# Kernel tuning notes

Hardware: AMD Instinct MI355X
Metric: run time of the kernel (lower is better)

The kernel has to match this reference:

```python
import jax, jax.numpy as jnp
import numpy as np

GROUPS = 32
GN_EPS = 1e-6
LN_EPS = 1e-5
HEADS = 8
DH = 40


def group_norm(x, w, b):
    # x: [B, C, H, W], GroupNorm over (C//GROUPS, H, W) within each group
    B, C, H, W = x.shape
    xg = x.reshape(B, GROUPS, C // GROUPS, H, W)
    mu = xg.mean(axis=(2, 3, 4), keepdims=True)
    var = xg.var(axis=(2, 3, 4), keepdims=True)
    xg = (xg - mu) * jax.lax.rsqrt(var + GN_EPS)
    return xg.reshape(B, C, H, W) * w[None, :, None, None] + b[None, :, None, None]


def layer_norm(x, w, b):
    mu = x.mean(axis=-1, keepdims=True)
    var = x.var(axis=-1, keepdims=True)
    return (x - mu) * jax.lax.rsqrt(var + LN_EPS) * w + b


def attention(x, ctx, wq, wk, wv, wo, bo):
    # x: [B, N, D], ctx: [B, M, Dc]; weights stored (in, out)
    B, N, _ = x.shape
    M = ctx.shape[1]
    q = (x @ wq).reshape(B, N, HEADS, DH)
    k = (ctx @ wk).reshape(B, M, HEADS, DH)
    v = (ctx @ wv).reshape(B, M, HEADS, DH)
    sim = jnp.einsum('bihd,bjhd->bhij', q, k) * (DH ** -0.5)
    attn = jax.nn.softmax(sim, axis=-1)
    out = jnp.einsum('bhij,bjhd->bihd', attn, v).reshape(B, N, HEADS * DH)
    return out @ wo + bo


def geglu_ff(x, w1, b1, w2, b2):
    h = x @ w1 + b1
    a, g = jnp.split(h, 2, axis=-1)
    return (a * jax.nn.gelu(g, approximate=False)) @ w2 + b2


def conv1x1(x, w, b):
    # w: [C_out, C_in]
    return jnp.einsum('bihw,oi->bohw', x, w) + b[None, :, None, None]


def reference(x, context, gn_w, gn_b, pin_w, pin_b,
              ln1_w, ln1_b, q1, k1, v1, o1_w, o1_b,
              ln2_w, ln2_b, q2, k2, v2, o2_w, o2_b,
              ln3_w, ln3_b, ff1_w, ff1_b, ff2_w, ff2_b,
              pout_w, pout_b):
    B, C, H, W = x.shape
    x_in = x
    h = group_norm(x, gn_w, gn_b)
    h = conv1x1(h, pin_w, pin_b)
    h = h.reshape(B, C, H * W).transpose(0, 2, 1)  # b (h w) c
    # BasicTransformerBlock
    h = attention(layer_norm(h, ln1_w, ln1_b), layer_norm(h, ln1_w, ln1_b), q1, k1, v1, o1_w, o1_b) + h
    h = attention(layer_norm(h, ln2_w, ln2_b), context, q2, k2, v2, o2_w, o2_b) + h
    h = geglu_ff(layer_norm(h, ln3_w, ln3_b), ff1_w, ff1_b, ff2_w, ff2_b) + h
    h = h.transpose(0, 2, 1).reshape(B, C, H, W)
    h = conv1x1(h, pout_w, pout_b)
    return h + x_in


def setup_inputs() -> dict:
    key = jax.random.key(0)
    ks = jax.random.split(key, 20)
    B, C, H, W = 1, 320, 64, 64
    CTX_N, CTX_D = 77, 768
    INNER, FFI = 320, 1280

    def n(k, shape, s=0.02):
        return jax.random.normal(k, shape, jnp.float32) * s

    return {
        'x': jax.random.normal(ks[0], (B, C, H, W), jnp.float32),
        'context': jax.random.normal(ks[1], (B, CTX_N, CTX_D), jnp.float32),
        'gn_w': jnp.ones((C,), jnp.float32), 'gn_b': jnp.zeros((C,), jnp.float32),
        'pin_w': n(ks[2], (INNER, C)), 'pin_b': jnp.zeros((INNER,), jnp.float32),
        'ln1_w': jnp.ones((INNER,), jnp.float32), 'ln1_b': jnp.zeros((INNER,), jnp.float32),
        'q1': n(ks[3], (INNER, INNER)), 'k1': n(ks[4], (INNER, INNER)), 'v1': n(ks[5], (INNER, INNER)),
        'o1_w': n(ks[6], (INNER, INNER)), 'o1_b': jnp.zeros((INNER,), jnp.float32),
        'ln2_w': jnp.ones((INNER,), jnp.float32), 'ln2_b': jnp.zeros((INNER,), jnp.float32),
        'q2': n(ks[7], (INNER, INNER)), 'k2': n(ks[8], (CTX_D, INNER)), 'v2': n(ks[9], (CTX_D, INNER)),
        'o2_w': n(ks[10], (INNER, INNER)), 'o2_b': jnp.zeros((INNER,), jnp.float32),
        'ln3_w': jnp.ones((INNER,), jnp.float32), 'ln3_b': jnp.zeros((INNER,), jnp.float32),
        'ff1_w': n(ks[11], (INNER, 2 * FFI)), 'ff1_b': jnp.zeros((2 * FFI,), jnp.float32),
        'ff2_w': n(ks[12], (FFI, INNER)), 'ff2_b': jnp.zeros((INNER,), jnp.float32),
        'pout_w': n(ks[13], (C, INNER)), 'pout_b': jnp.zeros((C,), jnp.float32),
    }
```

## Files before the change

kernel.cpp:

```cpp
#include <hip/hip_runtime.h>
#include <hip/hip_bf16.h>
#include <math.h>

#define N_SEQ  4096
#define DMODEL 320
#define NHEADS 8
#define DHEAD  40
#define CTXN   77
#define CTXD   768
#define FFI    1280

typedef short s8v __attribute__((ext_vector_type(8)));
typedef short s4v __attribute__((ext_vector_type(4)));
typedef float f4v __attribute__((ext_vector_type(4)));
typedef unsigned short u16;

static __device__ __forceinline__ u16 bf16u(float x) {
    unsigned u = __float_as_uint(x);
    return (u16)((u + 0x7FFFu + ((u >> 16) & 1u)) >> 16);
}
static __device__ __forceinline__ float b2f(u16 v) { return __uint_as_float((unsigned)v << 16); }
static __device__ __forceinline__ unsigned pack2(float a, float b) {
    return (unsigned)bf16u(a) | ((unsigned)bf16u(b) << 16);
}

#define GLD_LDS16(gp, lp) __builtin_amdgcn_global_load_lds( \
    (const __attribute__((address_space(1))) void*)(gp),    \
    (__attribute__((address_space(3))) void*)(lp), 16, 0, 0)

struct WC { const float* s; u16* d; int K, O, trans; };
struct WCs { WC a[12]; };
__global__ __launch_bounds__(256) void wcast2_k(WCs P) {
    __shared__ float tile[32][33];
    WC w = P.a[blockIdx.y];
    if (w.trans) {
        int ntk = w.K >> 5, nto = w.O >> 5;
        int tid = blockIdx.x;
        if (tid >= ntk * nto) return;
        int tk = tid % ntk, to = tid / ntk;
        int lr = threadIdx.x >> 5, lc = threadIdx.x & 31;
#pragma unroll
        for (int p = 0; p < 4; ++p) {
            int k = tk * 32 + p * 8 + lr;
            tile[p * 8 + lr][lc] = w.s[(size_t)k * w.O + to * 32 + lc];
        }
        __syncthreads();
#pragma unroll
        for (int p = 0; p < 4; ++p) {
            int o = to * 32 + p * 8 + lr;
            w.d[(size_t)o * w.K + tk * 32 + lc] = bf16u(tile[lc][p * 8 + lr]);
        }
    } else {
        int nel = w.K * w.O;
        for (int e = blockIdx.x * 256 + threadIdx.x; e < nel; e += gridDim.x * 256)
            w.d[e] = bf16u(w.s[e]);
    }
}

__global__ __launch_bounds__(256) void gn_stats_k(const float* __restrict__ x,
                                                  const float* __restrict__ gw, const float* __restrict__ gb,
                                                  float* __restrict__ sc, float* __restrict__ sh) {
    __shared__ float red[512];
    __shared__ float ms[2];
    int g = blockIdx.x, t = threadIdx.x;
    const float* xp = x + (size_t)g * 40960;
    float s = 0.f, ss = 0.f;
    for (int i = t; i < 40960; i += 256) { float v = xp[i]; s += v; ss += v * v; }
    red[t] = s; red[256 + t] = ss;
    __syncthreads();
    for (int st = 128; st > 0; st >>= 1) {
        if (t < st) { red[t] += red[t + st]; red[256 + t] += red[256 + t + st]; }
        __syncthreads();
    }
    if (t == 0) {
        float mean = red[0] / 40960.f;
        float var  = red[256] / 40960.f - mean * mean;
        ms[0] = mean; ms[1] = rsqrtf(var + 1e-6f);
    }
    __syncthreads();
    if (t < 10) {
        int c = g * 10 + t;
        float scv = gw[c] * ms[1];
        sc[c] = scv;
        sh[c] = gb[c] - ms[0] * scv;
    }
}

__global__ __launch_bounds__(256) void ln_stats_k(const float* __restrict__ in,
                                                  float* __restrict__ mu, float* __restrict__ rs) {
    int row = blockIdx.x * 4 + (threadIdx.x >> 6), l = threadIdx.x & 63;
    const float* p = in + (size_t)row * DMODEL;
    float s = 0.f, ss = 0.f;
#pragma unroll
    for (int j = 0; j < 5; ++j) { float v = p[l + 64 * j]; s += v; ss += v * v; }
    for (int o = 32; o > 0; o >>= 1) { s += __shfl_xor(s, o); ss += __shfl_xor(ss, o); }
    if (l == 0) {
        float mean = s * (1.f / 320.f);
        float var  = ss * (1.f / 320.f) - mean * mean;
        mu[row] = mean;
        rs[row] = rsqrtf(var + 1e-5f);
    }
}

struct GArg { const u16* Wt; const float* bias; float* outf; u16* outb; int ob_mode; };
#define GP 72
#define QSCALE 0.22811012f

template<int SITE>
__global__ __launch_bounds__(256) void gemm_t(const void* __restrict__ Av, int a_mode, int lda,
                                              const float* __restrict__ mu, const float* __restrict__ rs,
                                              const float* __restrict__ cw, const float* __restrict__ cb,
                                              GArg g0, GArg g1, GArg g2,
                                              const float* __restrict__ res,
                                              int Mrows, int K, int Oout, int obT_stride) {
    __shared__ __align__(16) u16 As[2][64 * GP];
    __shared__ __align__(16) u16 Wsm[2][64 * 64];
    const int t = threadIdx.x;
    const int w = t >> 6, lane = t & 63, c = lane & 15, quad = lane >> 4;
    const int o0 = blockIdx.x * 64, n0 = blockIdx.y * 64;
    GArg g = (blockIdx.z == 0) ? g0 : ((blockIdx.z == 1) ? g1 : g2);
    const f4v zero = {0.f, 0.f, 0.f, 0.f};
    f4v acc[4] = {zero, zero, zero, zero};
    const s8v z8 = {0, 0, 0, 0, 0, 0, 0, 0};
    const int nk = K >> 6;

    float fA[16];
    s8v bA0 = z8, bA1 = z8;

    const u16* gW0 = g.Wt + (size_t)(o0 + w * 16 + (lane >> 3)) * K + ((lane & 7) ^ (lane >> 3)) * 8;
    const u16* gW1 = gW0 + (size_t)8 * K;
    const int wdst = w * 1024;
    const int swb0 = 8 * (quad ^ (c & 7));
    const int swb1 = 8 * ((quad + 4) ^ (c & 7));

    auto gllW = [&](int b) {
        GLD_LDS16(gW0, &Wsm[b][wdst]);
        GLD_LDS16(gW1, &Wsm[b][wdst + 512]);
        gW0 += 64; gW1 += 64;
    };
    auto loadA = [&](int k0) {
        if (a_mode == 0) {
            const u16* A = (const u16*)Av;
            int i0 = t, i1 = t + 256;
            int nA = n0 + (i0 >> 3), nB = n0 + (i1 >> 3);
            bA0 = (nA < Mrows) ? *(const s8v*)(A + (size_t)nA * lda + k0 + (i0 & 7) * 8) : z8;
            bA1 = (nB < Mrows) ? *(const s8v*)(A + (size_t)nB * lda + k0 + (i1 & 7) * 8) : z8;
        } else if (a_mode == 1) {
            const float* A = (const float*)Av;
            int r = t >> 2, s16 = (t & 3) * 16;
            int n = n0 + r;
            if (n < Mrows) {
                const float* src = A + (size_t)n * lda + k0 + s16;
#pragma unroll
                for (int i = 0; i < 16; ++i) fA[i] = src[i];
            } else {
#pragma unroll
                for (int i = 0; i < 16; ++i) fA[i] = 0.f;
            }
        } else if (a_mode == 2) {
            const float* A = (const float*)Av;
#pragma unroll
            for (int j = 0; j < 16; ++j) {
                int e = t + 256 * j; int nn = e & 63, kk = e >> 6;
                int n = n0 + nn, kgl = k0 + kk;
                fA[j] = (n < Mrows) ? A[(size_t)kgl * lda + n] * cw[kgl] + cb[kgl] : 0.f;
            }
        } else if (a_mode == 3) {
            const float* A = (const float*)Av;
            int r = t >> 2, s16 = (t & 3) * 16;
            int n = n0 + r;
            if (n < Mrows) {
                const float* src = A + (size_t)n * lda + k0 + s16;
                const float* cwp = cw + k0 + s16;
                const float* cbp = cb + k0 + s16;
                float m_ = mu[n], rr = rs[n];
#pragma unroll
                for (int i = 0; i < 16; ++i) fA[i] = (src[i] - m_) * rr * cwp[i] + cbp[i];
            } else {
#pragma unroll
                for (int i = 0; i < 16; ++i) fA[i] = 0.f;
            }
        } else {
            const u16* Op = (const u16*)Av;
            const float* lp = mu;
            int r = t >> 2, s16 = (t & 3) * 16;
            int n = n0 + r;
            int ch0 = k0 + s16;
            int hdA = ch0 / 40;
            int hdB = (ch0 + 15) / 40;
            float invA = 1.f / (lp[(size_t)hdA * N_SEQ + n] + lp[(size_t)(8 + hdA) * N_SEQ + n]);
            float invB = (hdB == hdA) ? invA
                       : 1.f / (lp[(size_t)hdB * N_SEQ + n] + lp[(size_t)(8 + hdB) * N_SEQ + n]);
#pragma unroll
            for (int i = 0; i < 16; ++i) {
                int ch = ch0 + i;
                int hd = ch / 40;
                int d  = ch - hd * 40;
                float num = b2f(Op[((size_t)hd * N_SEQ + n) * DHEAD + d])
                          + b2f(Op[((size_t)(8 + hd) * N_SEQ + n) * DHEAD + d]);
                fA[i] = num * ((hd == hdA) ? invA : invB);
            }
        }
    };
    auto storeA = [&](int b) {
        if (a_mode == 0) {
            int i0 = t, i1 = t + 256;
            *(s8v*)&As[b][(i0 >> 3) * GP + (i0 & 7) * 8] = bA0;
            *(s8v*)&As[b][(i1 >> 3) * GP + (i1 & 7) * 8] = bA1;
        } else if (a_mode == 2) {
#pragma unroll
            for (int j = 0; j < 16; ++j) {
                int e = t + 256 * j; int nn = e & 63, kk = e >> 6;
                As[b][nn * GP + kk] = bf16u(fA[j]);
            }
        } else {
            int r = t >> 2, s16 = (t & 3) * 16;
            unsigned* dst = (unsigned*)&As[b][r * GP + s16];
#pragma unroll
            for (int i = 0; i < 8; ++i) dst[i] = pack2(fA[2 * i], fA[2 * i + 1]);
        }
    };

    gllW(0); loadA(0);
    storeA(0);
    __syncthreads();
    for (int k = 0; k < nk; ++k) {
        const int cur = k & 1;
        if (k + 1 < nk) { gllW(1 - cur); loadA((k + 1) << 6); }
        s8v a0 = *(const s8v*)&As[cur][(w * 16 + c) * GP + quad * 8];
        s8v a1 = *(const s8v*)&As[cur][(w * 16 + c) * GP + 32 + quad * 8];
#pragma unroll
        for (int nt = 0; nt < 4; ++nt) {
            s8v b0 = *(const s8v*)&Wsm[cur][(nt * 16 + c) * 64 + swb0];
            s8v b1 = *(const s8v*)&Wsm[cur][(nt * 16 + c) * 64 + swb1];
            acc[nt] = __builtin_amdgcn_mfma_f32_16x16x32_bf16(a0, b0, acc[nt], 0, 0, 0);
            acc[nt] = __builtin_amdgcn_mfma_f32_16x16x32_bf16(a1, b1, acc[nt], 0, 0, 0);
        }
        if (k + 1 < nk) { storeA(1 - cur); }
        __syncthreads();
    }
#pragma unroll
    for (int nt = 0; nt < 4; ++nt) {
        int o = o0 + nt * 16 + c;
        float vv[4];
#pragma unroll
        for (int r = 0; r < 4; ++r) vv[r] = acc[nt][r] + (g.bias ? g.bias[o] : 0.f);
        if (g.ob_mode == 3) {
            int nb = n0 + w * 16 + quad * 4;
            const float4 x4 = *(const float4*)(res + (size_t)o * obT_stride + nb);
            float4 o4 = make_float4(vv[0] + x4.x, vv[1] + x4.y, vv[2] + x4.z, vv[3] + x4.w);
            *(float4*)(g.outf + (size_t)o * obT_stride + nb) = o4;
        } else if (g.ob_mode == 4) {
#pragma unroll
            for (int r = 0; r < 4; ++r) {
                int n = n0 + w * 16 + quad * 4 + r;
                float vvv = vv[r];
                if (o < 320) vvv *= QSCALE;
                u16 bv = bf16u(vvv);
                if (o < 320)      g0.outb[(size_t)n * 320 + o] = bv;
                else if (o < 640) g1.outb[(size_t)n * 320 + (o - 320)] = bv;
                else              g2.outb[(size_t)(o - 640) * obT_stride + n] = bv;
            }
        } else {
#pragma unroll
            for (int r = 0; r < 4; ++r) {
                int n = n0 + w * 16 + quad * 4 + r;
                if (n >= Mrows) continue;
                float v = vv[r];
                if (res) v += res[(size_t)n * Oout + o];
                if (g.outf) g.outf[(size_t)n * Oout + o] = v;
                if (g.ob_mode == 1) g.outb[(size_t)n * Oout + o] = bf16u(v);
                else if (g.ob_mode == 2) g.outb[(size_t)o * obT_stride + n] = bf16u(v);
            }
        }
    }
}

__global__ __launch_bounds__(256) void gemm_gg(const float* __restrict__ A, int lda,
                                               const float* __restrict__ mu, const float* __restrict__ rs,
                                               const float* __restrict__ cw, const float* __restrict__ cb,
                                               const u16* __restrict__ Wt, const float* __restrict__ bias,
                                               u16* __restrict__ outb,
                                               int K, int Oout, int geglu_off) {
    __shared__ __align__(16) u16 As[64 * GP];
    __shared__ __align__(16) u16 Wsm[64 * GP];
    __shared__ __align__(16) u16 Wgm[64 * GP];
    const int t = threadIdx.x;
    const int w = t >> 6, lane = t & 63, c = lane & 15, quad = lane >> 4;
    const int o0 = blockIdx.x * 64, n0 = blockIdx.y * 64;
    const f4v zero = {0.f, 0.f, 0.f, 0.f};
    f4v acc[4]  = {zero, zero, zero, zero};
    f4v accg[4] = {zero, zero, zero, zero};
    const int nk = K >> 6;

    float fA[16];
    s8v wv0, wv1, gv0, gv1;

    auto loadWG = [&](int k0) {
        int i0 = t, i1 = t + 256;
        wv0 = *(const s8v*)(Wt + (size_t)(o0 + (i0 >> 3)) * K + k0 + (i0 & 7) * 8);
        wv1 = *(const s8v*)(Wt + (size_t)(o0 + (i1 >> 3)) * K + k0 + (i1 & 7) * 8);
        gv0 = *(const s8v*)(Wt + (size_t)(o0 + (i0 >> 3) + geglu_off) * K + k0 + (i0 & 7) * 8);
        gv1 = *(const s8v*)(Wt + (size_t)(o0 + (i1 >> 3) + geglu_off) * K + k0 + (i1 & 7) * 8);
    };
    auto storeWG = [&]() {
        int i0 = t, i1 = t + 256;
        *(s8v*)&Wsm[(i0 >> 3) * GP + (i0 & 7) * 8] = wv0;
        *(s8v*)&Wsm[(i1 >> 3) * GP + (i1 & 7) * 8] = wv1;
        *(s8v*)&Wgm[(i0 >> 3) * GP + (i0 & 7) * 8] = gv0;
        *(s8v*)&Wgm[(i1 >> 3) * GP + (i1 & 7) * 8] = gv1;
    };
    auto loadA = [&](int k0) {
        int r = t >> 2, s16 = (t & 3) * 16;
        int n = n0 + r;
        const float* src = A + (size_t)n * lda + k0 + s16;
        const float* cwp = cw + k0 + s16;
        const float* cbp = cb + k0 + s16;
        float m_ = mu[n], rr = rs[n];
#pragma unroll
        for (int i = 0; i < 16; ++i) fA[i] = (src[i] - m_) * rr * cwp[i] + cbp[i];
    };
    auto storeA = [&]() {
        int r = t >> 2, s16 = (t & 3) * 16;
        unsigned* dst = (unsigned*)&As[r * GP + s16];
#pragma unroll
        for (int i = 0; i < 8; ++i) dst[i] = pack2(fA[2 * i], fA[2 * i + 1]);
    };

    loadA(0); loadWG(0);
    storeA(); storeWG();
    __syncthreads();
    for (int k = 0; k < nk; ++k) {
        if (k + 1 < nk) { loadA((k + 1) << 6); loadWG((k + 1) << 6); }
        s8v a0 = *(const s8v*)&As[(w * 16 + c) * GP + quad * 8];
        s8v a1 = *(const s8v*)&As[(w * 16 + c) * GP + 32 + quad * 8];
#pragma unroll
        for (int nt = 0; nt < 4; ++nt) {
            s8v b0 = *(const s8v*)&Wsm[(nt * 16 + c) * GP + quad * 8];
            s8v b1 = *(const s8v*)&Wsm[(nt * 16 + c) * GP + 32 + quad * 8];
            acc[nt] = __builtin_amdgcn_mfma_f32_16x16x32_bf16(a0, b0, acc[nt], 0, 0, 0);
            acc[nt] = __builtin_amdgcn_mfma_f32_16x16x32_bf16(a1, b1, acc[nt], 0, 0, 0);
            s8v q0 = *(const s8v*)&Wgm[(nt * 16 + c) * GP + quad * 8];
            s8v q1 = *(const s8v*)&Wgm[(nt * 16 + c) * GP + 32 + quad * 8];
            accg[nt] = __builtin_amdgcn_mfma_f32_16x16x32_bf16(a0, q0, accg[nt], 0, 0, 0);
            accg[nt] = __builtin_amdgcn_mfma_f32_16x16x32_bf16(a1, q1, accg[nt], 0, 0, 0);
        }
        __syncthreads();
        if (k + 1 < nk) {
            storeA(); storeWG();
            __syncthreads();
        }
    }
#pragma unroll
    for (int nt = 0; nt < 4; ++nt) {
        int o = o0 + nt * 16 + c;
#pragma unroll
        for (int r = 0; r < 4; ++r) {
            int n = n0 + w * 16 + quad * 4 + r;
            float v = acc[nt][r] + bias[o];
            float gg = accg[nt][r] + bias[o + geglu_off];
            v = v * 0.5f * gg * (1.f + erff(gg * 0.70710678118654752f));
            outb[(size_t)n * Oout + o] = bf16u(v);
        }
    }
}

#define KSP 40
#define PSP 140
#define VP  136
__global__ __launch_bounds__(512) void attn_self10_k(const u16* __restrict__ qb, const u16* __restrict__ kb,
                                                     const u16* __restrict__ vt,
                                                     u16* __restrict__ Opart, float* __restrict__ lpart) {
    __shared__ __align__(16) u16 Ks[128 * KSP];
    __shared__ __align__(16) u16 Ps[128 * PSP];
    __shared__ __align__(16) u16 Vs[48 * VP];
    const int t = threadIdx.x;
    const int w = t >> 6, lane = t & 63, c = lane & 15, quad = lane >> 4;
    const int hd = blockIdx.y, ks = blockIdx.z;
    const int q0 = blockIdx.x * 128;
    const f4v zero = {0.f, 0.f, 0.f, 0.f};
    const s8v z8 = {0, 0, 0, 0, 0, 0, 0, 0};

    for (int i = t; i < 8 * VP / 2; i += 512) ((unsigned*)&Vs[40 * VP])[i] = 0u;
    __syncthreads();
    if (t < VP) Vs[40 * VP + t] = (u16)0x3F80;

    const u16* qrow = qb + (size_t)(q0 + w * 16 + c) * DMODEL + hd * DHEAD;
    s8v qa0 = *(const s8v*)(qrow + quad * 8);
    s8v qa1 = z8;
    if (quad == 0) qa1 = *(const s8v*)(qrow + 32);

    const int i0 = t, i2 = t + 512;
    const int r0 = i0 / 5, s0 = i0 - r0 * 5;
    const int r2 = (t < 128) ? i2 / 5 : r0, s2 = (t < 128) ? (i2 - (i2 / 5) * 5) : s0;
    const u16* kq0 = kb + (size_t)(ks * 2048 + r0) * DMODEL + hd * DHEAD + s0 * 8;
    const u16* kq2 = kb + (size_t)(ks * 2048 + r2) * DMODEL + hd * DHEAD + s2 * 8;
    u16* ksd0 = &Ks[r0 * KSP + s0 * 8];
    u16* ksd2 = &Ks[r2 * KSP + s2 * 8];
    const int d0 = i0 >> 4, g0v = i0 & 15;
    const int d2 = (t < 128) ? (i2 >> 4) : d0, g2v = (t < 128) ? (i2 & 15) : g0v;
    const u16* vq0 = vt + (size_t)(hd * DHEAD + d0) * N_SEQ + ks * 2048 + g0v * 8;
    const u16* vq2 = vt + (size_t)(hd * DHEAD + d2) * N_SEQ + ks * 2048 + g2v * 8;
    u16* vsd0 = &Vs[d0 * VP + g0v * 8];
    u16* vsd2 = &Vs[d2 * VP + g2v * 8];
    const size_t kadv = (size_t)128 * DMODEL;

    s8v kA = *(const s8v*)kq0, kC = *(const s8v*)kq2;
    s8v vA = *(const s8v*)vq0, vC = *(const s8v*)vq2;
    kq0 += kadv; kq2 += kadv;
    vq0 += 128;  vq2 += 128;

    f4v o0 = zero, o1 = zero, o2 = zero;

    for (int kt = 0; kt < 16; ++kt) {
        __syncthreads();
        *(s8v*)ksd0 = kA; *(s8v*)vsd0 = vA;
        if (t < 128) { *(s8v*)ksd2 = kC; *(s8v*)vsd2 = vC; }
        if (kt + 1 < 16) {
            kA = *(const s8v*)kq0; vA = *(const s8v*)vq0;
            if (t < 128) { kC = *(const s8v*)kq2; vC = *(const s8v*)vq2; }
            kq0 += kadv; kq2 += kadv;
            vq0 += 128;  vq2 += 128;
        }
        __syncthreads();

        f4v sarr[8];
#pragma unroll
        for (int nt = 0; nt < 8; ++nt) {
            const int kr = nt * 16 + c;
            s8v b0 = *(const s8v*)&Ks[kr * KSP + quad * 8];
            s8v b1 = z8;
            if (quad == 0) b1 = *(const s8v*)&Ks[kr * KSP + 32];
            f4v s = __builtin_amdgcn_mfma_f32_16x16x32_bf16(qa0, b0, zero, 0, 0, 0);
            s = __builtin_amdgcn_mfma_f32_16x16x32_bf16(qa1, b1, s, 0, 0, 0);
            sarr[nt] = s;
        }

        u16* psw = &Ps[(size_t)(w * 16 + quad * 4) * PSP + c];
#pragma unroll
        for (int reg = 0; reg < 8; ++reg) {
            const int colb = (reg >> 2) * 64 + (reg & 3) * 16;
#pragma unroll
            for (int r = 0; r < 4; ++r) {
                float pv = exp2f(sarr[reg][r]);
                psw[r * PSP + colb] = (u16)(__float_as_uint(pv) >> 16);
            }
        }

        const u16* prow = &Ps[(size_t)(w * 16 + c) * PSP];
#pragma unroll
        for (int h2 = 0; h2 < 2; ++h2) {
            s8v pa0, pa1;
            {
                s4v lo = *(const s4v*)(prow + h2 * 64 + quad * 8);
                s4v hi = *(const s4v*)(prow + h2 * 64 + quad * 8 + 4);
                pa0 = (s8v){lo[0], lo[1], lo[2], lo[3], hi[0], hi[1], hi[2], hi[3]};
                s4v lo2 = *(const s4v*)(prow + h2 * 64 + 32 + quad * 8);
                s4v hi2 = *(const s4v*)(prow + h2 * 64 + 32 + quad * 8 + 4);
                pa1 = (s8v){lo2[0], lo2[1], lo2[2], lo2[3], hi2[0], hi2[1], hi2[2], hi2[3]};
            }
            {
                s8v v0 = *(const s8v*)&Vs[(0 * 16 + c) * VP + h2 * 64 + quad * 8];
                s8v v1 = *(const s8v*)&Vs[(0 * 16 + c) * VP + h2 * 64 + 32 + quad * 8];
                o0 = __builtin_amdgcn_mfma_f32_16x16x32_bf16(pa0, v0, o0, 0, 0, 0);
                o0 = __builtin_amdgcn_mfma_f32_16x16x32_bf16(pa1, v1, o0, 0, 0, 0);
            }
            {
                s8v v0 = *(const s8v*)&Vs[(1 * 16 + c) * VP + h2 * 64 + quad * 8];
                s8v v1 = *(const s8v*)&Vs[(1 * 16 + c) * VP + h2 * 64 + 32 + quad * 8];
                o1 = __builtin_amdgcn_mfma_f32_16x16x32_bf16(pa0, v0, o1, 0, 0, 0);
                o1 = __builtin_amdgcn_mfma_f32_16x16x32_bf16(pa1, v1, o1, 0, 0, 0);
            }
            {
                s8v v0 = *(const s8v*)&Vs[(2 * 16 + c) * VP + h2 * 64 + quad * 8];
                s8v v1 = *(const s8v*)&Vs[(2 * 16 + c) * VP + h2 * 64 + 32 + quad * 8];
                o2 = __builtin_amdgcn_mfma_f32_16x16x32_bf16(pa0, v0, o2, 0, 0, 0);
                o2 = __builtin_amdgcn_mfma_f32_16x16x32_bf16(pa1, v1, o2, 0, 0, 0);
            }
        }
    }

    const size_t pb = (size_t)(ks * 8 + hd) * N_SEQ;
#pragma unroll
    for (int r = 0; r < 4; ++r) {
        int q = q0 + w * 16 + quad * 4 + r;
        u16* op = Opart + (pb + q) * DHEAD;
        op[c]      = bf16u(o0[r]);
        op[16 + c] = bf16u(o1[r]);
        if (c < 8) op[32 + c] = bf16u(o2[r]);
        if (c == 8) lpart[pb + q] = o2[r];
    }
}

__global__ __launch_bounds__(256) void attn_cross3_k(const u16* __restrict__ qb,
                                                     const u16* __restrict__ kb,
                                                     const u16* __restrict__ vt,
                                                     u16* __restrict__ outb) {
    __shared__ __align__(16) u16 KsPs[64 * PSP];
    __shared__ __align__(16) u16 Vs[48 * VP];
    const int t = threadIdx.x;
    const int w = t >> 6, lane = t & 63, c = lane & 15, quad = lane >> 4;
    const int hd = blockIdx.y;
    const int q0 = blockIdx.x * 64;
    const float SC2 = 0.15811388300841897f * 1.4426950408889634f;
    const f4v zero = {0.f, 0.f, 0.f, 0.f};
    const s8v z8 = {0, 0, 0, 0, 0, 0, 0, 0};

    for (int i = t; i < 48 * VP / 2; i += 256) ((unsigned*)Vs)[i] = 0u;
    __syncthreads();
    if (t < VP) Vs[40 * VP + t] = (u16)0x3F80;
    for (int i = t; i < 400; i += 256) {
        int d = i / 10, kc = i - d * 10;
        s8v v = *(const s8v*)(vt + (size_t)(hd * DHEAD + d) * 128 + kc * 8);
        if (kc == 9) { v[5] = 0; v[6] = 0; v[7] = 0; }
        *(s8v*)&Vs[d * VP + kc * 8] = v;
    }
    for (int i = t; i < 385; i += 256) {
        int r = i / 5, sg = i - r * 5;
        *(s8v*)&KsPs[r * KSP + sg * 8] = *(const s8v*)(kb + (size_t)r * DMODEL + hd * DHEAD + sg * 8);
    }
    const u16* qrow = qb + (size_t)(q0 + w * 16 + c) * DMODEL + hd * DHEAD;
    s8v qa0 = *(const s8v*)(qrow + quad * 8);
    s8v qa1 = z8;
    if (quad == 0) qa1 = *(const s8v*)(qrow + 32);
    __syncthreads();

    f4v sarr[5];
#pragma unroll
    for (int nt = 0; nt < 5; ++nt) {
        const int kr = nt * 16 + c;
        s8v b0 = *(const s8v*)&KsPs[kr * KSP + quad * 8];
        s8v b1 = z8;
        if (quad == 0) b1 = *(const s8v*)&KsPs[kr * KSP + 32];
        f4v s = __builtin_amdgcn_mfma_f32_16x16x32_bf16(qa0, b0, zero, 0, 0, 0);
        s = __builtin_amdgcn_mfma_f32_16x16x32_bf16(qa1, b1, s, 0, 0, 0);
        sarr[nt] = s;
    }
    __syncthreads();

    u16* psw = &KsPs[(size_t)(w * 16 + quad * 4) * PSP + c];
#pragma unroll
    for (int r = 0; r < 4; ++r) {
        float s4 = (c < 13) ? sarr[4][r] : -1e30f;
        float mx = fmaxf(fmaxf(fmaxf(sarr[0][r], sarr[1][r]), fmaxf(sarr[2][r], sarr[3][r])), s4);
        mx = fmaxf(mx, __shfl_xor(mx, 1));
        mx = fmaxf(mx, __shfl_xor(mx, 2));
        mx = fmaxf(mx, __shfl_xor(mx, 4));
        mx = fmaxf(mx, __shfl_xor(mx, 8));
#pragma unroll
        for (int nt = 0; nt < 4; ++nt)
            psw[r * PSP + nt * 16] = bf16u(exp2f((sarr[nt][r] - mx) * SC2));
        psw[r * PSP + 64] = (c < 13) ? bf16u(exp2f((s4 - mx) * SC2)) : (u16)0;
        psw[r * PSP + 80] = 0;
    }

    const u16* prow = &KsPs[(size_t)(w * 16 + c) * PSP];
    f4v o0 = zero, o1 = zero, o2 = zero;
#pragma unroll
    for (int ch = 0; ch < 3; ++ch) {
        s4v lo = *(const s4v*)(prow + ch * 32 + quad * 8);
        s4v hi = *(const s4v*)(prow + ch * 32 + quad * 8 + 4);
        s8v pa = (s8v){lo[0], lo[1], lo[2], lo[3], hi[0], hi[1], hi[2], hi[3]};
        s8v v0 = *(const s8v*)&Vs[(0 * 16 + c) * VP + ch * 32 + quad * 8];
        o0 = __builtin_amdgcn_mfma_f32_16x16x32_bf16(pa, v0, o0, 0, 0, 0);
        s8v v1 = *(const s8v*)&Vs[(1 * 16 + c) * VP + ch * 32 + quad * 8];
        o1 = __builtin_amdgcn_mfma_f32_16x16x32_bf16(pa, v1, o1, 0, 0, 0);
        s8v v2 = *(const s8v*)&Vs[(2 * 16 + c) * VP + ch * 32 + quad * 8];
        o2 = __builtin_amdgcn_mfma_f32_16x16x32_bf16(pa, v2, o2, 0, 0, 0);
    }

#pragma unroll
    for (int r = 0; r < 4; ++r) {
        float inv = 1.f / __shfl(o2[r], (lane & 48) | 8);
        int q = q0 + w * 16 + quad * 4 + r;
        u16* op = outb + (size_t)q * DMODEL + hd * DHEAD;
        op[c]      = bf16u(o0[r] * inv);
        op[16 + c] = bf16u(o1[r] * inv);
        if (c < 8) op[32 + c] = bf16u(o2[r] * inv);
    }
}

extern "C" void kernel_launch(void* const* d_in, const int* in_sizes, int n_in,
                              void* d_out, int out_size, void* d_ws, size_t ws_size,
                              hipStream_t stream) {
    const float* x      = (const float*)d_in[0];
    const float* ctx    = (const float*)d_in[1];
    const float* gn_w   = (const float*)d_in[2];
    const float* gn_b   = (const float*)d_in[3];
    const float* pin_w  = (const float*)d_in[4];
    const float* pin_b  = (const float*)d_in[5];
    const float* ln1_w  = (const float*)d_in[6];
    const float* ln1_b  = (const float*)d_in[7];
    const float* q1     = (const float*)d_in[8];
    const float* k1     = (const float*)d_in[9];
    const float* v1     = (const float*)d_in[10];
    const float* o1_w   = (const float*)d_in[11];
    const float* o1_b   = (const float*)d_in[12];
    const float* ln2_w  = (const float*)d_in[13];
    const float* ln2_b  = (const float*)d_in[14];
    const float* q2     = (const float*)d_in[15];
    const float* k2     = (const float*)d_in[16];
    const float* v2     = (const float*)d_in[17];
    const float* o2_w   = (const float*)d_in[18];
    const float* o2_b   = (const float*)d_in[19];
    const float* ln3_w  = (const float*)d_in[20];
    const float* ln3_b  = (const float*)d_in[21];
    const float* ff1_w  = (const float*)d_in[22];
    const float* ff1_b  = (const float*)d_in[23];
    const float* ff2_w  = (const float*)d_in[24];
    const float* ff2_b  = (const float*)d_in[25];
    const float* pout_w = (const float*)d_in[26];
    const float* pout_b = (const float*)d_in[27];
    float* out = (float*)d_out;

    char* base = (char*)d_ws;
    float* h     = (float*)(base);
    u16*   qb16  = (u16*)(base + 5242880);
    u16*   kb16  = (u16*)(base + 7864320);
    u16*   vt16  = (u16*)(base + 10485760);
    u16*   ao16  = (u16*)(base + 13107200);
    u16*   ffg16 = (u16*)(base + 5242880);
    u16*   wbase = (u16*)(base + 15728640);
    u16* pinT  = wbase;
    u16* q1T   = pinT  + 102400;
    u16* k1T   = q1T   + 102400;
    u16* v1T   = k1T   + 102400;
    u16* o1T   = v1T   + 102400;
    u16* q2T   = o1T   + 102400;
    u16* o2T   = q2T   + 102400;
    u16* k2T   = o2T   + 102400;
    u16* v2T   = k2T   + 245760;
    u16* ff1T  = v2T   + 245760;
    u16* ff2T  = ff1T  + 819200;
    u16* poutT = ff2T  + 409600;
    float* lnmu = (float*)(base + 20807680);
    float* lnrs = lnmu + 4096;
    u16*   k2b16 = (u16*)(lnrs + 4096);
    u16*   v2t16 = (u16*)(lnrs + 4096 + 25600);
    u16*   Opart = (u16*)(lnrs + 4096 + 51200);
    float* lpart = (float*)(Opart + (size_t)2 * 8 * 4096 * 40);
    float* gnsc  = lpart + 2 * 8 * 4096;
    float* gnsh  = gnsc + 320;

    WCs wd;
    wd.a[0]  = {pin_w,  pinT,  320,  320,  0};
    wd.a[1]  = {q1,     q1T,   320,  320,  1};
    wd.a[2]  = {k1,     k1T,   320,  320,  1};
    wd.a[3]  = {v1,     v1T,   320,  320,  1};
    wd.a[4]  = {o1_w,   o1T,   320,  320,  1};
    wd.a[5]  = {q2,     q2T,   320,  320,  1};
    wd.a[6]  = {o2_w,   o2T,   320,  320,  1};
    wd.a[7]  = {k2,     k2T,   768,  320,  1};
    wd.a[8]  = {v2,     v2T,   768,  320,  1};
    wd.a[9]  = {ff1_w,  ff1T,  320,  2560, 1};
    wd.a[10] = {ff2_w,  ff2T,  1280, 320,  1};
    wd.a[11] = {pout_w, poutT, 320,  320,  0};
    wcast2_k<<<dim3(800, 12), 256, 0, stream>>>(wd);

    GArg gz = {nullptr, nullptr, nullptr, nullptr, 0};

    gn_stats_k<<<32, 256, 0, stream>>>(x, gn_w, gn_b, gnsc, gnsh);
    {
        GArg g0 = {pinT, pin_b, h, nullptr, 0};
        gemm_t<0><<<dim3(5, 64, 1), 256, 0, stream>>>(x, 2, 4096, nullptr, nullptr, gnsc, gnsh,
                                                      g0, gz, gz, nullptr, 4096, 320, 320, 0);
    }
    ln_stats_k<<<1024, 256, 0, stream>>>(h, lnmu, lnrs);
    {
        GArg g0 = {q1T, nullptr, nullptr, qb16, 4};
        GArg g1 = {nullptr, nullptr, nullptr, kb16, 0};
        GArg g2 = {nullptr, nullptr, nullptr, vt16, 0};
        gemm_t<1><<<dim3(15, 64, 1), 256, 0, stream>>>(h, 3, 320, lnmu, lnrs, ln1_w, ln1_b,
                                                       g0, g1, g2, nullptr, 4096, 320, 960, 4096);
    }
    attn_self10_k<<<dim3(32, 8, 2), 512, 0, stream>>>(qb16, kb16, vt16, Opart, lpart);
    {
        GArg g0 = {o1T, o1_b, h, nullptr, 0};
        gemm_t<2><<<dim3(5, 64, 1), 256, 0, stream>>>(Opart, 4, 0, lpart, nullptr, nullptr, nullptr,
                                                      g0, gz, gz, h, 4096, 320, 320, 0);
    }
    ln_stats_k<<<1024, 256, 0, stream>>>(h, lnmu, lnrs);
    {
        GArg g0 = {q2T, nullptr, nullptr, qb16, 1};
        gemm_t<3><<<dim3(5, 64, 1), 256, 0, stream>>>(h, 3, 320, lnmu, lnrs, ln2_w, ln2_b,
                                                      g0, gz, gz, nullptr, 4096, 320, 320, 0);
    }
    {
        GArg g0 = {k2T, nullptr, nullptr, k2b16, 1};
        GArg g1 = {v2T, nullptr, nullptr, v2t16, 2};
        gemm_t<4><<<dim3(5, 2, 2), 256, 0, stream>>>(ctx, 1, 768, nullptr, nullptr, nullptr, nullptr,
                                                     g0, g1, gz, nullptr, 77, 768, 320, 128);
    }
    attn_cross3_k<<<dim3(64, 8), 256, 0, stream>>>(qb16, k2b16, v2t16, ao16);
    {
        GArg g0 = {o2T, o2_b, h, nullptr, 0};
        gemm_t<5><<<dim3(5, 64, 1), 256, 0, stream>>>(ao16, 0, 320, nullptr, nullptr, nullptr, nullptr,
                                                      g0, gz, gz, h, 4096, 320, 320, 0);
    }
    ln_stats_k<<<1024, 256, 0, stream>>>(h, lnmu, lnrs);
    gemm_gg<<<dim3(20, 64, 1), 256, 0, stream>>>(h, 320, lnmu, lnrs, ln3_w, ln3_b,
                                                 ff1T, ff1_b, ffg16, 320, 1280, 1280);
    {
        GArg g0 = {ff2T, ff2_b, h, nullptr, 0};
        gemm_t<6><<<dim3(5, 64, 1), 256, 0, stream>>>(ffg16, 0, 1280, nullptr, nullptr, nullptr, nullptr,
                                                      g0, gz, gz, h, 4096, 1280, 320, 0);
    }
    {
        GArg g0 = {poutT, pout_b, out, nullptr, 3};
        gemm_t<7><<<dim3(5, 64, 1), 256, 0, stream>>>(h, 1, 320, nullptr, nullptr, nullptr, nullptr,
                                                      g0, gz, gz, x, 4096, 320, 320, 4096);
    }
}
```

Measured before the change: 421.3 us.

## Materialize LayerNorm output as bf16 and double-buffer GEGLU GEMM with async weight loads

The LayerNorm stats kernel now writes fully normalized bf16 activations, so the downstream Q/KV/FF1 GEMMs read bf16 rows directly instead of re-normalizing fp32 inputs inside every output-column tile. The GEGLU GEMM is also reworked to use double-buffered LDS with direct global-to-LDS swizzled weight loads and a single barrier per k-step. The cost is an extra bf16 activation buffer write and read, and a larger LDS footprint in the GEGLU kernel, which may lower occupancy.

Result: slower. 482.5 us (+14.5%).

```diff
diff --git a/kernel.cpp b/kernel.cpp
--- a/kernel.cpp
+++ b/kernel.cpp
@@ -86,20 +86,22 @@
     }
 }
 
-__global__ __launch_bounds__(256) void ln_stats_k(const float* __restrict__ in,
-                                                  float* __restrict__ mu, float* __restrict__ rs) {
+__global__ __launch_bounds__(256) void ln_norm_k(const float* __restrict__ in,
+                                                 const float* __restrict__ lw, const float* __restrict__ lb,
+                                                 u16* __restrict__ out) {
     int row = blockIdx.x * 4 + (threadIdx.x >> 6), l = threadIdx.x & 63;
     const float* p = in + (size_t)row * DMODEL;
+    float v[5];
     float s = 0.f, ss = 0.f;
 #pragma unroll
-    for (int j = 0; j < 5; ++j) { float v = p[l + 64 * j]; s += v; ss += v * v; }
+    for (int j = 0; j < 5; ++j) { v[j] = p[l + 64 * j]; s += v[j]; ss += v[j] * v[j]; }
     for (int o = 32; o > 0; o >>= 1) { s += __shfl_xor(s, o); ss += __shfl_xor(ss, o); }
-    if (l == 0) {
-        float mean = s * (1.f / 320.f);
-        float var  = ss * (1.f / 320.f) - mean * mean;
-        mu[row] = mean;
-        rs[row] = rsqrtf(var + 1e-5f);
-    }
+    float mu = s * (1.f / 320.f);
+    float rs = rsqrtf(ss * (1.f / 320.f) - mu * mu + 1e-5f);
+    u16* op = out + (size_t)row * DMODEL;
+#pragma unroll
+    for (int j = 0; j < 5; ++j)
+        op[l + 64 * j] = bf16u((v[j] - mu) * rs * lw[l + 64 * j] + lb[l + 64 * j]);
 }
 
 struct GArg { const u16* Wt; const float* bias; float* outf; u16* outb; int ob_mode; };
@@ -165,21 +167,6 @@
                 int n = n0 + nn, kgl = k0 + kk;
                 fA[j] = (n < Mrows) ? A[(size_t)kgl * lda + n] * cw[kgl] + cb[kgl] : 0.f;
             }
-        } else if (a_mode == 3) {
-            const float* A = (const float*)Av;
-            int r = t >> 2, s16 = (t & 3) * 16;
-            int n = n0 + r;
-            if (n < Mrows) {
-                const float* src = A + (size_t)n * lda + k0 + s16;
-                const float* cwp = cw + k0 + s16;
-                const float* cbp = cb + k0 + s16;
-                float m_ = mu[n], rr = rs[n];
-#pragma unroll
-                for (int i = 0; i < 16; ++i) fA[i] = (src[i] - m_) * rr * cwp[i] + cbp[i];
-            } else {
-#pragma unroll
-                for (int i = 0; i < 16; ++i) fA[i] = 0.f;
-            }
         } else {
             const u16* Op = (const u16*)Av;
             const float* lp = mu;
@@ -276,15 +263,13 @@
     }
 }
 
-__global__ __launch_bounds__(256) void gemm_gg(const float* __restrict__ A, int lda,
-                                               const float* __restrict__ mu, const float* __restrict__ rs,
-                                               const float* __restrict__ cw, const float* __restrict__ cb,
+__global__ __launch_bounds__(256) void gemm_gg(const u16* __restrict__ A,
                                                const u16* __restrict__ Wt, const float* __restrict__ bias,
                                                u16* __restrict__ outb,
                                                int K, int Oout, int geglu_off) {
-    __shared__ __align__(16) u16 As[64 * GP];
-    __shared__ __align__(16) u16 Wsm[64 * GP];
-    __shared__ __align__(16) u16 Wgm[64 * GP];
+    __shared__ __align__(16) u16 As[2][64 * GP];
+    __shared__ __align__(16) u16 Wsm[2][64 * 64];
+    __shared__ __align__(16) u16 Wgm[2][64 * 64];
     const int t = threadIdx.x;
     const int w = t >> 6, lane = t & 63, c = lane & 15, quad = lane >> 4;
     const int o0 = blockIdx.x * 64, n0 = blockIdx.y * 64;
@@ -293,63 +278,54 @@
     f4v accg[4] = {zero, zero, zero, zero};
     const int nk = K >> 6;
 
-    float fA[16];
-    s8v wv0, wv1, gv0, gv1;
-
-    auto loadWG = [&](int k0) {
-        int i0 = t, i1 = t + 256;
-        wv0 = *(const s8v*)(Wt + (size_t)(o0 + (i0 >> 3)) * K + k0 + (i0 & 7) * 8);
-        wv1 = *(const s8v*)(Wt + (size_t)(o0 + (i1 >> 3)) * K + k0 + (i1 & 7) * 8);
-        gv0 = *(const s8v*)(Wt + (size_t)(o0 + (i0 >> 3) + geglu_off) * K + k0 + (i0 & 7) * 8);
-        gv1 = *(const s8v*)(Wt + (size_t)(o0 + (i1 >> 3) + geglu_off) * K + k0 + (i1 & 7) * 8);
-    };
-    auto storeWG = [&]() {
-        int i0 = t, i1 = t + 256;
-        *(s8v*)&Wsm[(i0 >> 3) * GP + (i0 & 7) * 8] = wv0;
-        *(s8v*)&Wsm[(i1 >> 3) * GP + (i1 & 7) * 8] = wv1;
-        *(s8v*)&Wgm[(i0 >> 3) * GP + (i0 & 7) * 8] = gv0;
-        *(s8v*)&Wgm[(i1 >> 3) * GP + (i1 & 7) * 8] = gv1;
+    s8v bA0, bA1;
+    const u16* gW0 = Wt + (size_t)(o0 + w * 16 + (lane >> 3)) * K + ((lane & 7) ^ (lane >> 3)) * 8;
+    const u16* gW1 = gW0 + (size_t)8 * K;
+    const u16* gG0 = gW0 + (size_t)geglu_off * K;
+    const u16* gG1 = gW1 + (size_t)geglu_off * K;
+    const int wdst = w * 1024;
+    const int swb0 = 8 * (quad ^ (c & 7));
+    const int swb1 = 8 * ((quad + 4) ^ (c & 7));
+
+    auto gllWG = [&](int b) {
+        GLD_LDS16(gW0, &Wsm[b][wdst]);
+        GLD_LDS16(gW1, &Wsm[b][wdst + 512]);
+        GLD_LDS16(gG0, &Wgm[b][wdst]);
+        GLD_LDS16(gG1, &Wgm[b][wdst + 512]);
+        gW0 += 64; gW1 += 64; gG0 += 64; gG1 += 64;
     };
     auto loadA = [&](int k0) {
-        int r = t >> 2, s16 = (t & 3) * 16;
-        int n = n0 + r;
-        const float* src = A + (size_t)n * lda + k0 + s16;
-        const float* cwp = cw + k0 + s16;
-        const float* cbp = cb + k0 + s16;
-        float m_ = mu[n], rr = rs[n];
-#pragma unroll
-        for (int i = 0; i < 16; ++i) fA[i] = (src[i] - m_) * rr * cwp[i] + cbp[i];
+        int i0 = t, i1 = t + 256;
+        bA0 = *(const s8v*)(A + (size_t)(n0 + (i0 >> 3)) * K + k0 + (i0 & 7) * 8);
+        bA1 = *(const s8v*)(A + (size_t)(n0 + (i1 >> 3)) * K + k0 + (i1 & 7) * 8);
     };
-    auto storeA = [&]() {
-        int r = t >> 2, s16 = (t & 3) * 16;
-        unsigned* dst = (unsigned*)&As[r * GP + s16];
-#pragma unroll
-        for (int i = 0; i < 8; ++i) dst[i] = pack2(fA[2 * i], fA[2 * i + 1]);
+    auto storeA = [&](int b) {
+        int i0 = t, i1 = t + 256;
+        *(s8v*)&As[b][(i0 >> 3) * GP + (i0 & 7) * 8] = bA0;
+        *(s8v*)&As[b][(i1 >> 3) * GP + (i1 & 7) * 8] = bA1;
     };
 
-    loadA(0); loadWG(0);
-    storeA(); storeWG();
+    gllWG(0); loadA(0);
+    storeA(0);
     __syncthreads();
     for (int k = 0; k < nk; ++k) {
-        if (k + 1 < nk) { loadA((k + 1) << 6); loadWG((k + 1) << 6); }
-        s8v a0 = *(const s8v*)&As[(w * 16 + c) * GP + quad * 8];
-        s8v a1 = *(const s8v*)&As[(w * 16 + c) * GP + 32 + quad * 8];
+        const int cur = k & 1;
+        if (k + 1 < nk) { gllWG(1 - cur); loadA((k + 1) << 6); }
+        s8v a0 = *(const s8v*)&As[cur][(w * 16 + c) * GP + quad * 8];
+        s8v a1 = *(const s8v*)&As[cur][(w * 16 + c) * GP + 32 + quad * 8];
 #pragma unroll
         for (int nt = 0; nt < 4; ++nt) {
-            s8v b0 = *(const s8v*)&Wsm[(nt * 16 + c) * GP + quad * 8];
-            s8v b1 = *(const s8v*)&Wsm[(nt * 16 + c) * GP + 32 + quad * 8];
+            s8v b0 = *(const s8v*)&Wsm[cur][(nt * 16 + c) * 64 + swb0];
+            s8v b1 = *(const s8v*)&Wsm[cur][(nt * 16 + c) * 64 + swb1];
             acc[nt] = __builtin_amdgcn_mfma_f32_16x16x32_bf16(a0, b0, acc[nt], 0, 0, 0);
             acc[nt] = __builtin_amdgcn_mfma_f32_16x16x32_bf16(a1, b1, acc[nt], 0, 0, 0);
-            s8v q0 = *(const s8v*)&Wgm[(nt * 16 + c) * GP + quad * 8];
-            s8v q1 = *(const s8v*)&Wgm[(nt * 16 + c) * GP + 32 + quad * 8];
+            s8v q0 = *(const s8v*)&Wgm[cur][(nt * 16 + c) * 64 + swb0];
+            s8v q1 = *(const s8v*)&Wgm[cur][(nt * 16 + c) * 64 + swb1];
             accg[nt] = __builtin_amdgcn_mfma_f32_16x16x32_bf16(a0, q0, accg[nt], 0, 0, 0);
             accg[nt] = __builtin_amdgcn_mfma_f32_16x16x32_bf16(a1, q1, accg[nt], 0, 0, 0);
         }
+        if (k + 1 < nk) { storeA(1 - cur); }
         __syncthreads();
-        if (k + 1 < nk) {
-            storeA(); storeWG();
-            __syncthreads();
-        }
     }
 #pragma unroll
     for (int nt = 0; nt < 4; ++nt) {
@@ -619,6 +595,7 @@
     u16*   kb16  = (u16*)(base + 7864320);
     u16*   vt16  = (u16*)(base + 10485760);
     u16*   ao16  = (u16*)(base + 13107200);
+    u16*   hb16  = (u16*)(base + 13107200);
     u16*   ffg16 = (u16*)(base + 5242880);
     u16*   wbase = (u16*)(base + 15728640);
     u16* pinT  = wbase;
@@ -665,12 +642,12 @@
         gemm_t<0><<<dim3(5, 64, 1), 256, 0, stream>>>(x, 2, 4096, nullptr, nullptr, gnsc, gnsh,
                                                       g0, gz, gz, nullptr, 4096, 320, 320, 0);
     }
-    ln_stats_k<<<1024, 256, 0, stream>>>(h, lnmu, lnrs);
+    ln_norm_k<<<1024, 256, 0, stream>>>(h, ln1_w, ln1_b, hb16);
     {
         GArg g0 = {q1T, nullptr, nullptr, qb16, 4};
         GArg g1 = {nullptr, nullptr, nullptr, kb16, 0};
         GArg g2 = {nullptr, nullptr, nullptr, vt16, 0};
-        gemm_t<1><<<dim3(15, 64, 1), 256, 0, stream>>>(h, 3, 320, lnmu, lnrs, ln1_w, ln1_b,
+        gemm_t<1><<<dim3(15, 64, 1), 256, 0, stream>>>(hb16, 0, 320, nullptr, nullptr, nullptr, nullptr,
                                                        g0, g1, g2, nullptr, 4096, 320, 960, 4096);
     }
     attn_self10_k<<<dim3(32, 8, 2), 512, 0, stream>>>(qb16, kb16, vt16, Opart, lpart);
@@ -679,10 +656,10 @@
         gemm_t<2><<<dim3(5, 64, 1), 256, 0, stream>>>(Opart, 4, 0, lpart, nullptr, nullptr, nullptr,
                                                       g0, gz, gz, h, 4096, 320, 320, 0);
     }
-    ln_stats_k<<<1024, 256, 0, stream>>>(h, lnmu, lnrs);
+    ln_norm_k<<<1024, 256, 0, stream>>>(h, ln2_w, ln2_b, hb16);
     {
         GArg g0 = {q2T, nullptr, nullptr, qb16, 1};
-        gemm_t<3><<<dim3(5, 64, 1), 256, 0, stream>>>(h, 3, 320, lnmu, lnrs, ln2_w, ln2_b,
+        gemm_t<3><<<dim3(5, 64, 1), 256, 0, stream>>>(hb16, 0, 320, nullptr, nullptr, nullptr, nullptr,
                                                       g0, gz, gz, nullptr, 4096, 320, 320, 0);
     }
     {
@@ -697,9 +674,8 @@
         gemm_t<5><<<dim3(5, 64, 1), 256, 0, stream>>>(ao16, 0, 320, nullptr, nullptr, nullptr, nullptr,
                                                       g0, gz, gz, h, 4096, 320, 320, 0);
     }
-    ln_stats_k<<<1024, 256, 0, stream>>>(h, lnmu, lnrs);
-    gemm_gg<<<dim3(20, 64, 1), 256, 0, stream>>>(h, 320, lnmu, lnrs, ln3_w, ln3_b,
-                                                 ff1T, ff1_b, ffg16, 320, 1280, 1280);
+    ln_norm_k<<<1024, 256, 0, stream>>>(h, ln3_w, ln3_b, hb16);
+    gemm_gg<<<dim3(20, 64, 1), 256, 0, stream>>>(hb16, ff1T, ff1_b, ffg16, 320, 1280, 1280);
     {
         GArg g0 = {ff2T, ff2_b, h, nullptr, 0};
         gemm_t<6><<<dim3(5, 64, 1), 256, 0, stream>>>(ffg16, 0, 1280, nullptr, nullptr, nullptr, nullptr,
```
